# Performance work log

Hardware: AMD Instinct MI355X
Metric: run time of the kernel (lower is better)

The kernel has to match this reference:

```python
import jax, jax.numpy as jnp
import numpy as np

HIDDEN = 2048
N_HEADS = 32
N_KV = 4
HEAD_DIM = 128
EPS = 1e-6
THETA = 1e6
B, S = 2, 2048


def setup_inputs() -> dict:
    key = jax.random.key(0)
    k1, k2, k3 = jax.random.split(key, 3)
    hidden_states = jax.random.normal(k1, (B, S, HIDDEN), dtype=jnp.float32)
    positions = jnp.broadcast_to(jnp.arange(S, dtype=jnp.int32), (B, S))
    w_qkv = jax.random.normal(k2, ((N_HEADS + 2 * N_KV) * HEAD_DIM, HIDDEN), dtype=jnp.float32) * 0.02
    w_o = jax.random.normal(k3, (HIDDEN, N_HEADS * HEAD_DIM), dtype=jnp.float32) * 0.02
    q_norm_w = jnp.ones((HEAD_DIM,), dtype=jnp.float32)
    k_norm_w = jnp.ones((HEAD_DIM,), dtype=jnp.float32)
    return {"hidden_states": hidden_states, "positions": positions,
            "w_qkv": w_qkv, "w_o": w_o, "q_norm_w": q_norm_w, "k_norm_w": k_norm_w}


def _rms_norm(x, w):
    # x: [..., HEAD_DIM]
    var = jnp.mean(x * x, axis=-1, keepdims=True)
    return x * jax.lax.rsqrt(var + EPS) * w


def _rope(x, positions):
    # NEOX-style rotary. x: [B,S,H,D], positions: [B,S]
    half = HEAD_DIM // 2
    inv_freq = 1.0 / (THETA ** (jnp.arange(0, half, dtype=jnp.float32) / half))
    ang = positions.astype(jnp.float32)[..., None] * inv_freq  # [B,S,half]
    cos = jnp.cos(ang)[:, :, None, :]
    sin = jnp.sin(ang)[:, :, None, :]
    x1, x2 = x[..., :half], x[..., half:]
    return jnp.concatenate([x1 * cos - x2 * sin, x2 * cos + x1 * sin], axis=-1)


def reference(hidden_states, positions, w_qkv, w_o, q_norm_w, k_norm_w):
    q_size = N_HEADS * HEAD_DIM
    kv_size = N_KV * HEAD_DIM
    qkv = jnp.einsum('bsh,oh->bso', hidden_states, w_qkv)
    q = qkv[..., :q_size].reshape(B, S, N_HEADS, HEAD_DIM)
    k = qkv[..., q_size:q_size + kv_size].reshape(B, S, N_KV, HEAD_DIM)
    v = qkv[..., q_size + kv_size:].reshape(B, S, N_KV, HEAD_DIM)
    # per-head RMSNorm then RoPE
    q = _rope(_rms_norm(q, q_norm_w), positions)
    k = _rope(_rms_norm(k, k_norm_w), positions)
    rep = N_HEADS // N_KV
    k = jnp.repeat(k, rep, axis=2)
    v = jnp.repeat(v, rep, axis=2)
    scale = HEAD_DIM ** -0.5
    scores = jnp.einsum('bqhd,bkhd->bhqk', q, k) * scale
    causal = jnp.tril(jnp.ones((S, S), dtype=bool))
    scores = jnp.where(causal, scores, jnp.finfo(scores.dtype).min)
    probs = jax.nn.softmax(scores, axis=-1)
    attn = jnp.einsum('bhqk,bkhd->bqhd', probs, v).reshape(B, S, N_HEADS * HEAD_DIM)
    return jnp.einsum('bsa,ha->bsh', attn, w_o)
```

## Files before the change

### kernel.cpp

```cpp
#include <hip/hip_runtime.h>
#include <cstdint>

#define SEQ 2048
#define BATCH 2
#define NTOK 4096
#define HID 2048
#define NH 32
#define NKV 4
#define HD 128
#define QKV_O 5120

typedef __attribute__((ext_vector_type(8))) short short8;
typedef __attribute__((ext_vector_type(8))) unsigned short u16x8;
typedef __attribute__((ext_vector_type(4))) unsigned short u16x4;
typedef __attribute__((ext_vector_type(4))) float f32x4;

__device__ __forceinline__ float bf2f(unsigned short u) {
  union { unsigned int i; float f; } v; v.i = ((unsigned int)u) << 16; return v.f;
}
__device__ __forceinline__ unsigned short f2bf(float f) {
  union { float f; unsigned int i; } v; v.f = f;
  unsigned int r = v.i + 0x7FFFu + ((v.i >> 16) & 1u);
  return (unsigned short)(r >> 16);
}

__device__ __forceinline__ void load_lds16(const void* g, void* l) {
  __builtin_amdgcn_global_load_lds((const __attribute__((address_space(1))) unsigned int*)g,
                                   (__attribute__((address_space(3))) unsigned int*)l, 16, 0, 0);
}

__device__ __forceinline__ float exp2n(float x) { return __builtin_amdgcn_exp2f(x); }

__global__ __launch_bounds__(256) void convert5(
    const float* __restrict__ s0, unsigned short* __restrict__ d0, int n0,
    const float* __restrict__ s1, unsigned short* __restrict__ d1, int n1,
    const float* __restrict__ s2, unsigned short* __restrict__ d2, int n2,
    const float* __restrict__ s3, unsigned short* __restrict__ d3, int n3,
    const float* __restrict__ s4, unsigned short* __restrict__ d4, int n4_) {
  const float* s; unsigned short* d; int n;
  switch (blockIdx.y) {
    case 0: s = s0; d = d0; n = n0; break;
    case 1: s = s1; d = d1; n = n1; break;
    case 2: s = s2; d = d2; n = n2; break;
    case 3: s = s3; d = d3; n = n3; break;
    default: s = s4; d = d4; n = n4_; break;
  }
  int i = blockIdx.x * blockDim.x + threadIdx.x;
  int stride = gridDim.x * blockDim.x;
  for (; i < n; i += stride) {
    f32x4 v = *(const f32x4*)(s + 4 * (size_t)i);
    u16x4 o;
    o.x = f2bf(v.x); o.y = f2bf(v.y); o.z = f2bf(v.z); o.w = f2bf(v.w);
    *(u16x4*)(d + 4 * (size_t)i) = o;
  }
}

template <bool OUT_F32>
__global__ __launch_bounds__(512, 2) void gemm256(
    const unsigned short* __restrict__ A, const unsigned short* __restrict__ B,
    void* __restrict__ Cv, int lda, int ldb, int ldc, int Kloop) {
  __shared__ alignas(16) unsigned short As[2][256 * 64];
  __shared__ alignas(16) unsigned short Bs[2][256 * 64];

  const int t = threadIdx.x;
  const int lane = t & 63, w = t >> 6;
  const int fr = lane & 15, g = lane >> 4;
  const int wm = w >> 2, wn = w & 3;
  const size_t m0 = (size_t)blockIdx.y * 256;
  const size_t n0 = (size_t)blockIdx.x * 256;

  const int srow = w * 8 + (lane >> 3);
  const int sch = (lane & 7) ^ ((lane >> 3) & 7);
  const unsigned short* gA[4];
  const unsigned short* gB[4];
#pragma unroll
  for (int i = 0; i < 4; i++) {
    gA[i] = A + (m0 + i * 64 + srow) * (size_t)lda + sch * 8;
    gB[i] = B + (n0 + i * 64 + srow) * (size_t)ldb + sch * 8;
  }

  auto stage = [&](int k0, int bi) {
#pragma unroll
    for (int i = 0; i < 4; i++) {
      load_lds16(gA[i] + k0, &As[bi][(i * 512 + w * 64) * 8]);
      load_lds16(gB[i] + k0, &Bs[bi][(i * 512 + w * 64) * 8]);
    }
  };

  f32x4 acc[8][4] = {};
  stage(0, 0);

  const int nk = Kloop / 64;
  for (int kt = 0; kt < nk; kt++) {
    const int cur = kt & 1;
    asm volatile("s_waitcnt vmcnt(0)" ::: "memory");
    __builtin_amdgcn_s_barrier();
    __builtin_amdgcn_sched_barrier(0);
    if (kt + 1 < nk) stage((kt + 1) * 64, cur ^ 1);

    const unsigned short* Ac = As[cur];
    const unsigned short* Bc = Bs[cur];

    short8 bfr[4][2];
#pragma unroll
    for (int nf = 0; nf < 4; nf++) {
      const int row = wn * 64 + nf * 16 + fr;
#pragma unroll
      for (int s = 0; s < 2; s++)
        bfr[nf][s] = *(const short8*)&Bc[row * 64 + (((s * 4 + g) ^ (fr & 7)) * 8)];
    }
    __builtin_amdgcn_s_setprio(1);
#pragma unroll
    for (int mf = 0; mf < 8; mf++) {
      const int row = wm * 128 + mf * 16 + fr;
      short8 af0 = *(const short8*)&Ac[row * 64 + (((0 + g) ^ (fr & 7)) * 8)];
      short8 af1 = *(const short8*)&Ac[row * 64 + (((4 + g) ^ (fr & 7)) * 8)];
#pragma unroll
      for (int nf = 0; nf < 4; nf++) {
        acc[mf][nf] = __builtin_amdgcn_mfma_f32_16x16x32_bf16(af0, bfr[nf][0], acc[mf][nf], 0, 0, 0);
        acc[mf][nf] = __builtin_amdgcn_mfma_f32_16x16x32_bf16(af1, bfr[nf][1], acc[mf][nf], 0, 0, 0);
      }
    }
    __builtin_amdgcn_s_setprio(0);
  }

#pragma unroll
  for (int mf = 0; mf < 8; mf++)
#pragma unroll
    for (int nf = 0; nf < 4; nf++) {
      size_t row = m0 + wm * 128 + mf * 16 + g * 4;
      size_t col = n0 + wn * 64 + nf * 16 + fr;
#pragma unroll
      for (int r = 0; r < 4; r++) {
        if (OUT_F32) ((float*)Cv)[(row + r) * ldc + col] = acc[mf][nf][r];
        else ((unsigned short*)Cv)[(row + r) * ldc + col] = f2bf(acc[mf][nf][r]);
      }
    }
}

__global__ __launch_bounds__(512, 2) void gemm256x128(
    const unsigned short* __restrict__ A, const unsigned short* __restrict__ B,
    float* __restrict__ C, int lda, int ldb, int ldc, int Kloop) {
  __shared__ alignas(16) unsigned short As[2][256 * 64];
  __shared__ alignas(16) unsigned short Bs[2][128 * 64];

  const int t = threadIdx.x;
  const int lane = t & 63, w = t >> 6;
  const int fr = lane & 15, g = lane >> 4;
  const int wm = w >> 1, wn = w & 1;
  const size_t m0 = (size_t)blockIdx.y * 256;
  const size_t n0 = (size_t)blockIdx.x * 128;

  const int srow = t >> 3;
  const int sch = (t & 7) ^ ((t >> 3) & 7);
  const unsigned short* gA[4];
  const unsigned short* gB[2];
#pragma unroll
  for (int i = 0; i < 4; i++)
    gA[i] = A + (m0 + i * 64 + srow) * (size_t)lda + sch * 8;
#pragma unroll
  for (int i = 0; i < 2; i++)
    gB[i] = B + (n0 + i * 64 + srow) * (size_t)ldb + sch * 8;

  auto stage = [&](int k0, int bi) {
#pragma unroll
    for (int i = 0; i < 4; i++)
      load_lds16(gA[i] + k0, &As[bi][(i * 512 + w * 64) * 8]);
#pragma unroll
    for (int i = 0; i < 2; i++)
      load_lds16(gB[i] + k0, &Bs[bi][(i * 512 + w * 64) * 8]);
  };

  f32x4 acc[4][4] = {};
  stage(0, 0);

  const int nk = Kloop / 64;
  for (int kt = 0; kt < nk; kt++) {
    const int cur = kt & 1;
    asm volatile("s_waitcnt vmcnt(0)" ::: "memory");
    __builtin_amdgcn_s_barrier();
    __builtin_amdgcn_sched_barrier(0);
    if (kt + 1 < nk) stage((kt + 1) * 64, cur ^ 1);

    const unsigned short* Ac = As[cur];
    const unsigned short* Bc = Bs[cur];

    short8 bfr[4][2];
#pragma unroll
    for (int nf = 0; nf < 4; nf++) {
      const int row = wn * 64 + nf * 16 + fr;
#pragma unroll
      for (int s = 0; s < 2; s++)
        bfr[nf][s] = *(const short8*)&Bc[row * 64 + (((s * 4 + g) ^ (fr & 7)) * 8)];
    }
    __builtin_amdgcn_s_setprio(1);
#pragma unroll
    for (int mf = 0; mf < 4; mf++) {
      const int row = wm * 64 + mf * 16 + fr;
      short8 af0 = *(const short8*)&Ac[row * 64 + (((0 + g) ^ (fr & 7)) * 8)];
      short8 af1 = *(const short8*)&Ac[row * 64 + (((4 + g) ^ (fr & 7)) * 8)];
#pragma unroll
      for (int nf = 0; nf < 4; nf++) {
        acc[mf][nf] = __builtin_amdgcn_mfma_f32_16x16x32_bf16(af0, bfr[nf][0], acc[mf][nf], 0, 0, 0);
        acc[mf][nf] = __builtin_amdgcn_mfma_f32_16x16x32_bf16(af1, bfr[nf][1], acc[mf][nf], 0, 0, 0);
      }
    }
    __builtin_amdgcn_s_setprio(0);
  }

#pragma unroll
  for (int mf = 0; mf < 4; mf++)
#pragma unroll
    for (int nf = 0; nf < 4; nf++) {
      size_t row = m0 + wm * 64 + mf * 16 + g * 4;
      size_t col = n0 + wn * 64 + nf * 16 + fr;
#pragma unroll
      for (int r = 0; r < 4; r++)
        C[(row + r) * ldc + col] = acc[mf][nf][r];
    }
}

template <bool OUT_F32>
__global__ __launch_bounds__(256) void gemm_bt_bf16(
    const unsigned short* __restrict__ A, const unsigned short* __restrict__ B,
    void* __restrict__ Cv, int lda, int ldb, int ldc, int K) {
  __shared__ alignas(16) unsigned short As[128 * 32];
  __shared__ alignas(16) unsigned short Bs[128 * 32];

  const int t    = threadIdx.x;
  const int lane = t & 63;
  const int w    = t >> 6;
  const int wm   = (w >> 1) * 64;
  const int wn   = (w & 1) * 64;
  const size_t m0 = (size_t)blockIdx.y * 128;
  const size_t n0 = (size_t)blockIdx.x * 128;

  f32x4 acc[4][4] = {};

  const int srow = w * 32 + (lane >> 2);
  const int scol = (lane & 3) * 8;
  const unsigned short* gA0 = &A[(m0 + srow) * (size_t)lda + scol];
  const unsigned short* gA1 = gA0 + 16 * (size_t)lda;
  const unsigned short* gB0 = &B[(n0 + srow) * (size_t)ldb + scol];
  const unsigned short* gB1 = gB0 + 16 * (size_t)ldb;
  unsigned short* lA0 = &As[(w * 32) * 32];
  unsigned short* lA1 = &As[(w * 32 + 16) * 32];
  unsigned short* lB0 = &Bs[(w * 32) * 32];
  unsigned short* lB1 = &Bs[(w * 32 + 16) * 32];

  const int fr = lane & 15;
  const int kb = (lane >> 4) * 8;

  for (int k0 = 0; k0 < K; k0 += 32) {
    load_lds16(gA0 + k0, lA0);
    load_lds16(gA1 + k0, lA1);
    load_lds16(gB0 + k0, lB0);
    load_lds16(gB1 + k0, lB1);
    __syncthreads();
    short8 af[4], bf[4];
#pragma unroll
    for (int mt = 0; mt < 4; mt++) af[mt] = *(const short8*)&As[(wm + mt * 16 + fr) * 32 + kb];
#pragma unroll
    for (int nt = 0; nt < 4; nt++) bf[nt] = *(const short8*)&Bs[(wn + nt * 16 + fr) * 32 + kb];
#pragma unroll
    for (int mt = 0; mt < 4; mt++)
#pragma unroll
      for (int nt = 0; nt < 4; nt++)
        acc[mt][nt] = __builtin_amdgcn_mfma_f32_16x16x32_bf16(af[mt], bf[nt], acc[mt][nt], 0, 0, 0);
    __syncthreads();
  }

  const int r4 = (lane >> 4) * 4;
  const int cc = lane & 15;
#pragma unroll
  for (int mt = 0; mt < 4; mt++)
#pragma unroll
    for (int nt = 0; nt < 4; nt++) {
      size_t row = m0 + wm + mt * 16 + r4;
      size_t col = n0 + wn + nt * 16 + cc;
#pragma unroll
      for (int r = 0; r < 4; r++) {
        if (OUT_F32) ((float*)Cv)[(row + r) * ldc + col] = acc[mt][nt][r];
        else ((unsigned short*)Cv)[(row + r) * ldc + col] = f2bf(acc[mt][nt][r]);
      }
    }
}

__global__ __launch_bounds__(64) void rope_tab(const int* __restrict__ pos,
                                               float2* __restrict__ tab) {
  const int tok = blockIdx.x;
  const int j = threadIdx.x;
  float p = (float)pos[tok];
  float inv_freq = expf((float)j * (-13.815510557964274f / 64.0f));
  float ang = p * inv_freq;
  float2 cs; cs.x = cosf(ang); cs.y = sinf(ang);
  tab[tok * 64 + j] = cs;
}

__global__ __launch_bounds__(256) void normrope_tv(
    unsigned short* __restrict__ qkv, const float2* __restrict__ tab,
    const unsigned short* __restrict__ qw, const unsigned short* __restrict__ kw,
    unsigned short* __restrict__ vt) {
  __shared__ alignas(16) unsigned short Vs[64][136];
  const int bid = blockIdx.x;
  const int t = threadIdx.x;

  if (bid < 9 * NTOK) {
    const int wv = t >> 6, lane = t & 63;
    const int hh = bid % 9;
    const int tok = bid / 9;
    const int h = hh * 4 + wv;
    const unsigned short* w = (h < NH) ? qw : kw;
    const size_t src = (size_t)tok * QKV_O + (size_t)h * HD;

    float x1 = bf2f(qkv[src + lane]);
    float x2 = bf2f(qkv[src + lane + 64]);
    float ss = x1 * x1 + x2 * x2;
#pragma unroll
    for (int off = 32; off; off >>= 1) ss += __shfl_xor(ss, off);
    float r = rsqrtf(ss * (1.0f / 128.0f) + 1e-6f);
    float n1 = x1 * r * bf2f(w[lane]);
    float n2 = x2 * r * bf2f(w[lane + 64]);

    float2 cs = tab[tok * 64 + lane];
    qkv[src + lane]      = f2bf(n1 * cs.x - n2 * cs.y);
    qkv[src + lane + 64] = f2bf(n2 * cs.x + n1 * cs.y);
  } else {
    const int r = bid - 9 * NTOK;
    const int tile = r & 31, kvh = (r >> 5) & 3, b = r >> 7;
    const int k0 = tile * 64;
    const int voff = (NH + NKV) * HD + kvh * HD;
    {
      const int row = t >> 2, cb = (t & 3) * 8;
      const size_t gb = (size_t)(b * SEQ + k0 + row) * QKV_O + voff;
#pragma unroll
      for (int i = 0; i < 4; i++)
        *(uint4*)&Vs[row][cb + 32 * i] = *(const uint4*)&qkv[gb + cb + 32 * i];
    }
    __syncthreads();
    const int d = t >> 1, half = t & 1;
    const size_t ob = ((size_t)((b * NKV + kvh) * HD + d)) * SEQ + k0 + half * 32;
#pragma unroll
    for (int i = 0; i < 4; i++) {
      u16x8 vv;
#pragma unroll
      for (int j = 0; j < 8; j++) vv[j] = Vs[half * 32 + i * 8 + j][d];
      *(u16x8*)&vt[ob + i * 8] = vv;
    }
  }
}

__global__ __launch_bounds__(512, 4) void flash_mfma(unsigned short* __restrict__ qkv,
                                                     const unsigned short* __restrict__ vt) {
  __shared__ alignas(16) unsigned short Kbuf[2][64 * 128];
  __shared__ alignas(16) unsigned short Vbuf[2][128 * 64];
  __shared__ alignas(16) unsigned short Ps[8][16 * 64];

  const int p = (int)blockIdx.x;
  const int h = blockIdx.y, b = blockIdx.z;
  const int t = threadIdx.x;
  const int lane = t & 63, w = t >> 6;
  const int c = lane & 15, g = lane >> 4;
  const int kvh = h >> 3;
  const int koff = NH * HD + kvh * HD;
  const float scale2 = 0.12751745f;
  const int swz = c & 7;
  const int nqt = SEQ / 128;

  const int rK0 = t >> 4,         jK0 = (t & 15) ^ (rK0 & 15);
  const int rK1 = (t + 512) >> 4, jK1 = ((t + 512) & 15) ^ (rK1 & 15);
  const int dV0 = t >> 3,         jV0 = (t & 7) ^ (dV0 & 7);
  const int dV1 = (t + 512) >> 3, jV1 = ((t + 512) & 7) ^ (dV1 & 7);
  const unsigned short* gK0 = qkv + (size_t)(b * SEQ + rK0) * QKV_O + koff + jK0 * 8;
  const unsigned short* gK1 = qkv + (size_t)(b * SEQ + rK1) * QKV_O + koff + jK1 * 8;
  const unsigned short* gV0 = vt + ((size_t)(b * NKV + kvh) * HD + dV0) * SEQ + jV0 * 8;
  const unsigned short* gV1 = vt + ((size_t)(b * NKV + kvh) * HD + dV1) * SEQ + jV1 * 8;

  auto stage = [&](int k0s, int bi) {
    load_lds16(gK0 + (size_t)k0s * QKV_O, &Kbuf[bi][(w * 64) * 8]);
    load_lds16(gK1 + (size_t)k0s * QKV_O, &Kbuf[bi][(w * 64 + 512) * 8]);
    load_lds16(gV0 + k0s, &Vbuf[bi][(w * 64) * 8]);
    load_lds16(gV1 + k0s, &Vbuf[bi][(w * 64 + 512) * 8]);
  };

  for (int job = 0; job < 2; job++) {
    const int qt = job == 0 ? (nqt - 1 - p) : p;
    const int q0 = qt * 128;
    const int nkt = 2 * qt + 2;

    stage(0, 0);

    short8 qf[4];
    {
      const size_t qr = (size_t)(b * SEQ + q0 + w * 16 + c) * QKV_O + (size_t)h * HD;
#pragma unroll
      for (int ks = 0; ks < 4; ks++)
        qf[ks] = *(const short8*)&qkv[qr + ks * 32 + g * 8];
    }

    f32x4 O[8] = {};
    float m_i = -1e30f, l_i = 0.0f;

    for (int kt = 0; kt < nkt; kt++) {
      const int cur = kt & 1;
      asm volatile("s_waitcnt vmcnt(0)" ::: "memory");
      __builtin_amdgcn_s_barrier();
      __builtin_amdgcn_sched_barrier(0);
      if (kt + 1 < nkt) stage((kt + 1) * 64, cur ^ 1);

      const unsigned short* Kc = Kbuf[cur];
      const unsigned short* Vc = Vbuf[cur];

      f32x4 sc[4];
#pragma unroll
      for (int mt = 0; mt < 4; mt++) sc[mt] = (f32x4){0.f, 0.f, 0.f, 0.f};
      __builtin_amdgcn_s_setprio(1);
#pragma unroll
      for (int ks = 0; ks < 4; ks++) {
#pragma unroll
        for (int mt = 0; mt < 4; mt++) {
          short8 kf = *(const short8*)&Kc[(mt * 16 + c) * 128 + (((ks * 4 + g) ^ c) * 8)];
          sc[mt] = __builtin_amdgcn_mfma_f32_16x16x32_bf16(kf, qf[ks], sc[mt], 0, 0, 0);
        }
      }
      __builtin_amdgcn_s_setprio(0);

      const int k0 = kt * 64;
      const int qrow = q0 + w * 16 + c;
      const bool need_mask = (k0 + 63 > q0 + w * 16);
#pragma unroll
      for (int mt = 0; mt < 4; mt++)
#pragma unroll
        for (int r = 0; r < 4; r++) {
          float s = sc[mt][r];
          if (need_mask && (k0 + mt * 16 + g * 4 + r > qrow)) s = -3.0e38f;
          sc[mt][r] = s;
        }
      float ma = fmaxf(fmaxf(sc[0][0], sc[0][1]), sc[0][2]);
      float mb = fmaxf(fmaxf(sc[0][3], sc[1][0]), sc[1][1]);
      float mc = fmaxf(fmaxf(sc[1][2], sc[1][3]), sc[2][0]);
      float md = fmaxf(fmaxf(sc[2][1], sc[2][2]), sc[2][3]);
      float me = fmaxf(fmaxf(sc[3][0], sc[3][1]), sc[3][2]);
      float mx = fmaxf(fmaxf(fmaxf(ma, mb), fmaxf(mc, md)), fmaxf(me, sc[3][3]));
      mx = fmaxf(mx, __shfl_xor(mx, 16));
      mx = fmaxf(mx, __shfl_xor(mx, 32));
      float mx2 = mx * scale2;

      if (!__all(mx2 - m_i <= 11.54156f)) {
        float m_new = fmaxf(m_i, mx2);
        float alpha = exp2n(m_i - m_new);
        f32x4 a4;
#pragma unroll
        for (int r = 0; r < 4; r++) a4[r] = __shfl(alpha, g * 4 + r);
#pragma unroll
        for (int nt = 0; nt < 8; nt++)
#pragma unroll
          for (int r = 0; r < 4; r++) O[nt][r] *= a4[r];
        l_i *= alpha;
        m_i = m_new;
      }

      float psum = 0.0f;
#pragma unroll
      for (int mt = 0; mt < 4; mt++) {
        float pv[4];
#pragma unroll
        for (int r = 0; r < 4; r++) {
          pv[r] = exp2n(__builtin_fmaf(sc[mt][r], scale2, -m_i));
          psum += pv[r];
        }
        unsigned int pk0, pk1;
        asm("v_cvt_pk_bf16_f32 %0, %1, %2" : "=v"(pk0) : "v"(pv[0]), "v"(pv[1]));
        asm("v_cvt_pk_bf16_f32 %0, %1, %2" : "=v"(pk1) : "v"(pv[2]), "v"(pv[3]));
        uint2 pk; pk.x = pk0; pk.y = pk1;
        *(uint2*)&Ps[w][c * 64 + (((mt * 2 + (g >> 1)) ^ swz) * 8) + (g & 1) * 4] = pk;
      }
      psum += __shfl_xor(psum, 16);
      psum += __shfl_xor(psum, 32);
      l_i += psum;

      __builtin_amdgcn_s_setprio(1);
#pragma unroll
      for (int ks = 0; ks < 2; ks++) {
        short8 pf = *(const short8*)&Ps[w][c * 64 + (((ks * 4 + g) ^ swz) * 8)];
#pragma unroll
        for (int nt = 0; nt < 8; nt++) {
          short8 vf = *(const short8*)&Vc[(nt * 16 + c) * 64 + (((ks * 4 + g) ^ swz) * 8)];
          O[nt] = __builtin_amdgcn_mfma_f32_16x16x32_bf16(pf, vf, O[nt], 0, 0, 0);
        }
      }
      __builtin_amdgcn_s_setprio(0);
    }

    f32x4 l4;
#pragma unroll
    for (int r = 0; r < 4; r++) l4[r] = __shfl(l_i, g * 4 + r);
    f32x4 li;
#pragma unroll
    for (int r = 0; r < 4; r++) li[r] = 1.0f / l4[r];
#pragma unroll
    for (int nt = 0; nt < 8; nt++)
#pragma unroll
      for (int r = 0; r < 4; r++) {
        size_t addr = (size_t)(b * SEQ + q0 + w * 16 + g * 4 + r) * QKV_O + h * HD + nt * 16 + c;
        qkv[addr] = f2bf(O[nt][r] * li[r]);
      }
  }
}

extern "C" void kernel_launch(void* const* d_in, const int* in_sizes, int n_in,
                              void* d_out, int out_size, void* d_ws, size_t ws_size,
                              hipStream_t stream) {
  const float* hidden_f = (const float*)d_in[0];
  const int* positions  = (const int*)d_in[1];
  const float* wqkv_f   = (const float*)d_in[2];
  const float* wo_f     = (const float*)d_in[3];
  const float* qn_f     = (const float*)d_in[4];
  const float* kn_f     = (const float*)d_in[5];
  float* out            = (float*)d_out;

  char* ws = (char*)d_ws;
  unsigned short* hidden_c = (unsigned short*)ws;
  unsigned short* wqkv_c   = (unsigned short*)(ws + 16777216);
  unsigned short* wo_c     = (unsigned short*)(ws + 37748736);
  unsigned short* qn_c     = (unsigned short*)(ws + 54525952);
  unsigned short* kn_c     = (unsigned short*)(ws + 54526208);
  unsigned short* qkv      = (unsigned short*)(ws + 54526464);
  unsigned short* vt_g     = (unsigned short*)(ws + 96469504);
  float2* rtab             = (float2*)ws;

  convert5<<<dim3(512, 5), 256, 0, stream>>>(
      hidden_f, hidden_c, NTOK * HID / 4,
      wqkv_f, wqkv_c, QKV_O * HID / 4,
      wo_f, wo_c, HID * NH * HD / 4,
      qn_f, qn_c, HD / 4,
      kn_f, kn_c, HD / 4);

  gemm256<false><<<dim3(NH * HD / 256, NTOK / 256), 512, 0, stream>>>(
      hidden_c, wqkv_c, qkv, HID, HID, QKV_O, HID);
  gemm_bt_bf16<false><<<dim3(2 * NKV * HD / 128, NTOK / 128), 256, 0, stream>>>(
      hidden_c, wqkv_c + (size_t)(NH * HD) * HID, qkv + NH * HD, HID, HID, QKV_O, HID);
  rope_tab<<<NTOK, 64, 0, stream>>>(positions, rtab);
  normrope_tv<<<9 * NTOK + 256, 256, 0, stream>>>(qkv, rtab, qn_c, kn_c, vt_g);
  flash_mfma<<<dim3(SEQ / 256, NH, BATCH), 512, 0, stream>>>(qkv, vt_g);
  gemm256x128<<<dim3(HID / 128, NTOK / 256), 512, 0, stream>>>(
      qkv, wo_c, out, QKV_O, NH * HD, HID, NH * HD);
}
```

Baseline: 464.7 us.

## Shrink flash KV tile to 32 and launch one q-tile per block

The flash attention kernel drops the paired-job scheme, where each block handled a long and a short causal q-tile. It now launches one block per 128-row q-tile, ordered longest first, and halves the K/V tile from 64 to 32 keys. LDS use shrinks enough that the launch bounds now ask for 8 blocks per CU instead of 4, which may raise occupancy and shorten per-step latency. In exchange it pays twice as many barriers and loop iterations, loses the load balancing the pairing gave, and may face register pressure under the tighter bound.

```diff
diff --git a/kernel.cpp b/kernel.cpp
--- a/kernel.cpp
+++ b/kernel.cpp
@@ -350,13 +350,13 @@
   }
 }
 
-__global__ __launch_bounds__(512, 4) void flash_mfma(unsigned short* __restrict__ qkv,
+__global__ __launch_bounds__(512, 8) void flash_mfma(unsigned short* __restrict__ qkv,
                                                      const unsigned short* __restrict__ vt) {
-  __shared__ alignas(16) unsigned short Kbuf[2][64 * 128];
-  __shared__ alignas(16) unsigned short Vbuf[2][128 * 64];
-  __shared__ alignas(16) unsigned short Ps[8][16 * 64];
-
-  const int p = (int)blockIdx.x;
+  __shared__ alignas(16) unsigned short Kbuf[2][32 * 128];
+  __shared__ alignas(16) unsigned short Vbuf[2][128 * 32];
+  __shared__ alignas(16) unsigned short Ps[8][16 * 32];
+
+  const int qt = 15 - (int)blockIdx.x;
   const int h = blockIdx.y, b = blockIdx.z;
   const int t = threadIdx.x;
   const int lane = t & 63, w = t >> 6;
@@ -364,148 +364,133 @@
   const int kvh = h >> 3;
   const int koff = NH * HD + kvh * HD;
   const float scale2 = 0.12751745f;
-  const int swz = c & 7;
-  const int nqt = SEQ / 128;
-
-  const int rK0 = t >> 4,         jK0 = (t & 15) ^ (rK0 & 15);
-  const int rK1 = (t + 512) >> 4, jK1 = ((t + 512) & 15) ^ (rK1 & 15);
-  const int dV0 = t >> 3,         jV0 = (t & 7) ^ (dV0 & 7);
-  const int dV1 = (t + 512) >> 3, jV1 = ((t + 512) & 7) ^ (dV1 & 7);
-  const unsigned short* gK0 = qkv + (size_t)(b * SEQ + rK0) * QKV_O + koff + jK0 * 8;
-  const unsigned short* gK1 = qkv + (size_t)(b * SEQ + rK1) * QKV_O + koff + jK1 * 8;
-  const unsigned short* gV0 = vt + ((size_t)(b * NKV + kvh) * HD + dV0) * SEQ + jV0 * 8;
-  const unsigned short* gV1 = vt + ((size_t)(b * NKV + kvh) * HD + dV1) * SEQ + jV1 * 8;
+  const int swz3 = c & 3;
+  const int q0 = qt * 128;
+  const int nkt = 4 * qt + 4;
+
+  const int rK = t >> 4, jK = (t & 15) ^ (rK & 15);
+  const int dV = t >> 2, jV = (t & 3) ^ (dV & 3);
+  const unsigned short* gK = qkv + (size_t)(b * SEQ + rK) * QKV_O + koff + jK * 8;
+  const unsigned short* gV = vt + ((size_t)(b * NKV + kvh) * HD + dV) * SEQ + jV * 8;
 
   auto stage = [&](int k0s, int bi) {
-    load_lds16(gK0 + (size_t)k0s * QKV_O, &Kbuf[bi][(w * 64) * 8]);
-    load_lds16(gK1 + (size_t)k0s * QKV_O, &Kbuf[bi][(w * 64 + 512) * 8]);
-    load_lds16(gV0 + k0s, &Vbuf[bi][(w * 64) * 8]);
-    load_lds16(gV1 + k0s, &Vbuf[bi][(w * 64 + 512) * 8]);
+    load_lds16(gK + (size_t)k0s * QKV_O, &Kbuf[bi][(w * 64) * 8]);
+    load_lds16(gV + k0s, &Vbuf[bi][(w * 64) * 8]);
   };
 
-  for (int job = 0; job < 2; job++) {
-    const int qt = job == 0 ? (nqt - 1 - p) : p;
-    const int q0 = qt * 128;
-    const int nkt = 2 * qt + 2;
-
-    stage(0, 0);
-
-    short8 qf[4];
+  stage(0, 0);
+
+  short8 qf[4];
+  {
+    const size_t qr = (size_t)(b * SEQ + q0 + w * 16 + c) * QKV_O + (size_t)h * HD;
+#pragma unroll
+    for (int ks = 0; ks < 4; ks++)
+      qf[ks] = *(const short8*)&qkv[qr + ks * 32 + g * 8];
+  }
+
+  f32x4 O[8] = {};
+  float m_i = -1e30f, l_i = 0.0f;
+
+  for (int kt = 0; kt < nkt; kt++) {
+    const int cur = kt & 1;
+    asm volatile("s_waitcnt vmcnt(0)" ::: "memory");
+    __builtin_amdgcn_s_barrier();
+    __builtin_amdgcn_sched_barrier(0);
+    if (kt + 1 < nkt) stage((kt + 1) * 32, cur ^ 1);
+
+    const unsigned short* Kc = Kbuf[cur];
+    const unsigned short* Vc = Vbuf[cur];
+
+    f32x4 sc[2];
+#pragma unroll
+    for (int mt = 0; mt < 2; mt++) sc[mt] = (f32x4){0.f, 0.f, 0.f, 0.f};
+    __builtin_amdgcn_s_setprio(1);
+#pragma unroll
+    for (int ks = 0; ks < 4; ks++) {
+#pragma unroll
+      for (int mt = 0; mt < 2; mt++) {
+        short8 kf = *(const short8*)&Kc[(mt * 16 + c) * 128 + (((ks * 4 + g) ^ c) * 8)];
+        sc[mt] = __builtin_amdgcn_mfma_f32_16x16x32_bf16(kf, qf[ks], sc[mt], 0, 0, 0);
+      }
+    }
+    __builtin_amdgcn_s_setprio(0);
+
+    const int k0 = kt * 32;
+    const int qrow = q0 + w * 16 + c;
+    const bool need_mask = (k0 + 31 > q0 + w * 16);
+#pragma unroll
+    for (int mt = 0; mt < 2; mt++)
+#pragma unroll
+      for (int r = 0; r < 4; r++) {
+        float s = sc[mt][r];
+        if (need_mask && (k0 + mt * 16 + g * 4 + r > qrow)) s = -3.0e38f;
+        sc[mt][r] = s;
+      }
+    float ma = fmaxf(fmaxf(sc[0][0], sc[0][1]), sc[0][2]);
+    float mb = fmaxf(fmaxf(sc[0][3], sc[1][0]), sc[1][1]);
+    float mx = fmaxf(fmaxf(ma, mb), fmaxf(sc[1][2], sc[1][3]));
+    mx = fmaxf(mx, __shfl_xor(mx, 16));
+    mx = fmaxf(mx, __shfl_xor(mx, 32));
+    float mx2 = mx * scale2;
+
+    if (!__all(mx2 - m_i <= 11.54156f)) {
+      float m_new = fmaxf(m_i, mx2);
+      float alpha = exp2n(m_i - m_new);
+      f32x4 a4;
+#pragma unroll
+      for (int r = 0; r < 4; r++) a4[r] = __shfl(alpha, g * 4 + r);
+#pragma unroll
+      for (int nt = 0; nt < 8; nt++)
+#pragma unroll
+        for (int r = 0; r < 4; r++) O[nt][r] *= a4[r];
+      l_i *= alpha;
+      m_i = m_new;
+    }
+
+    float psum = 0.0f;
+#pragma unroll
+    for (int mt = 0; mt < 2; mt++) {
+      float pv[4];
+#pragma unroll
+      for (int r = 0; r < 4; r++) {
+        pv[r] = exp2n(__builtin_fmaf(sc[mt][r], scale2, -m_i));
+        psum += pv[r];
+      }
+      unsigned int pk0, pk1;
+      asm("v_cvt_pk_bf16_f32 %0, %1, %2" : "=v"(pk0) : "v"(pv[0]), "v"(pv[1]));
+      asm("v_cvt_pk_bf16_f32 %0, %1, %2" : "=v"(pk1) : "v"(pv[2]), "v"(pv[3]));
+      uint2 pk; pk.x = pk0; pk.y = pk1;
+      *(uint2*)&Ps[w][c * 32 + (((mt * 2 + (g >> 1)) ^ swz3) * 8) + (g & 1) * 4] = pk;
+    }
+    psum += __shfl_xor(psum, 16);
+    psum += __shfl_xor(psum, 32);
+    l_i += psum;
+
+    __builtin_amdgcn_s_setprio(1);
     {
-      const size_t qr = (size_t)(b * SEQ + q0 + w * 16 + c) * QKV_O + (size_t)h * HD;
-#pragma unroll
-      for (int ks = 0; ks < 4; ks++)
-        qf[ks] = *(const short8*)&qkv[qr + ks * 32 + g * 8];
-    }
-
-    f32x4 O[8] = {};
-    float m_i = -1e30f, l_i = 0.0f;
-
-    for (int kt = 0; kt < nkt; kt++) {
-      const int cur = kt & 1;
-      asm volatile("s_waitcnt vmcnt(0)" ::: "memory");
-      __builtin_amdgcn_s_barrier();
-      __builtin_amdgcn_sched_barrier(0);
-      if (kt + 1 < nkt) stage((kt + 1) * 64, cur ^ 1);
-
-      const unsigned short* Kc = Kbuf[cur];
-      const unsigned short* Vc = Vbuf[cur];
-
-      f32x4 sc[4];
-#pragma unroll
-      for (int mt = 0; mt < 4; mt++) sc[mt] = (f32x4){0.f, 0.f, 0.f, 0.f};
-      __builtin_amdgcn_s_setprio(1);
-#pragma unroll
-      for (int ks = 0; ks < 4; ks++) {
-#pragma unroll
-        for (int mt = 0; mt < 4; mt++) {
-          short8 kf = *(const short8*)&Kc[(mt * 16 + c) * 128 + (((ks * 4 + g) ^ c) * 8)];
-          sc[mt] = __builtin_amdgcn_mfma_f32_16x16x32_bf16(kf, qf[ks], sc[mt], 0, 0, 0);
-        }
-      }
-      __builtin_amdgcn_s_setprio(0);
-
-      const int k0 = kt * 64;
-      const int qrow = q0 + w * 16 + c;
-      const bool need_mask = (k0 + 63 > q0 + w * 16);
-#pragma unroll
-      for (int mt = 0; mt < 4; mt++)
-#pragma unroll
-        for (int r = 0; r < 4; r++) {
-          float s = sc[mt][r];
-          if (need_mask && (k0 + mt * 16 + g * 4 + r > qrow)) s = -3.0e38f;
-          sc[mt][r] = s;
-        }
-      float ma = fmaxf(fmaxf(sc[0][0], sc[0][1]), sc[0][2]);
-      float mb = fmaxf(fmaxf(sc[0][3], sc[1][0]), sc[1][1]);
-      float mc = fmaxf(fmaxf(sc[1][2], sc[1][3]), sc[2][0]);
-      float md = fmaxf(fmaxf(sc[2][1], sc[2][2]), sc[2][3]);
-      float me = fmaxf(fmaxf(sc[3][0], sc[3][1]), sc[3][2]);
-      float mx = fmaxf(fmaxf(fmaxf(ma, mb), fmaxf(mc, md)), fmaxf(me, sc[3][3]));
-      mx = fmaxf(mx, __shfl_xor(mx, 16));
-      mx = fmaxf(mx, __shfl_xor(mx, 32));
-      float mx2 = mx * scale2;
-
-      if (!__all(mx2 - m_i <= 11.54156f)) {
-        float m_new = fmaxf(m_i, mx2);
-        float alpha = exp2n(m_i - m_new);
-        f32x4 a4;
-#pragma unroll
-        for (int r = 0; r < 4; r++) a4[r] = __shfl(alpha, g * 4 + r);
-#pragma unroll
-        for (int nt = 0; nt < 8; nt++)
-#pragma unroll
-          for (int r = 0; r < 4; r++) O[nt][r] *= a4[r];
-        l_i *= alpha;
-        m_i = m_new;
-      }
-
-      float psum = 0.0f;
-#pragma unroll
-      for (int mt = 0; mt < 4; mt++) {
-        float pv[4];
-#pragma unroll
-        for (int r = 0; r < 4; r++) {
-          pv[r] = exp2n(__builtin_fmaf(sc[mt][r], scale2, -m_i));
-          psum += pv[r];
-        }
-        unsigned int pk0, pk1;
-        asm("v_cvt_pk_bf16_f32 %0, %1, %2" : "=v"(pk0) : "v"(pv[0]), "v"(pv[1]));
-        asm("v_cvt_pk_bf16_f32 %0, %1, %2" : "=v"(pk1) : "v"(pv[2]), "v"(pv[3]));
-        uint2 pk; pk.x = pk0; pk.y = pk1;
-        *(uint2*)&Ps[w][c * 64 + (((mt * 2 + (g >> 1)) ^ swz) * 8) + (g & 1) * 4] = pk;
-      }
-      psum += __shfl_xor(psum, 16);
-      psum += __shfl_xor(psum, 32);
-      l_i += psum;
-
-      __builtin_amdgcn_s_setprio(1);
-#pragma unroll
-      for (int ks = 0; ks < 2; ks++) {
-        short8 pf = *(const short8*)&Ps[w][c * 64 + (((ks * 4 + g) ^ swz) * 8)];
-#pragma unroll
-        for (int nt = 0; nt < 8; nt++) {
-          short8 vf = *(const short8*)&Vc[(nt * 16 + c) * 64 + (((ks * 4 + g) ^ swz) * 8)];
-          O[nt] = __builtin_amdgcn_mfma_f32_16x16x32_bf16(pf, vf, O[nt], 0, 0, 0);
-        }
-      }
-      __builtin_amdgcn_s_setprio(0);
-    }
-
-    f32x4 l4;
-#pragma unroll
-    for (int r = 0; r < 4; r++) l4[r] = __shfl(l_i, g * 4 + r);
-    f32x4 li;
-#pragma unroll
-    for (int r = 0; r < 4; r++) li[r] = 1.0f / l4[r];
-#pragma unroll
-    for (int nt = 0; nt < 8; nt++)
-#pragma unroll
-      for (int r = 0; r < 4; r++) {
-        size_t addr = (size_t)(b * SEQ + q0 + w * 16 + g * 4 + r) * QKV_O + h * HD + nt * 16 + c;
-        qkv[addr] = f2bf(O[nt][r] * li[r]);
-      }
-  }
+      short8 pf = *(const short8*)&Ps[w][c * 32 + ((g ^ swz3) * 8)];
+#pragma unroll
+      for (int nt = 0; nt < 8; nt++) {
+        short8 vf = *(const short8*)&Vc[(nt * 16 + c) * 32 + ((g ^ swz3) * 8)];
+        O[nt] = __builtin_amdgcn_mfma_f32_16x16x32_bf16(pf, vf, O[nt], 0, 0, 0);
+      }
+    }
+    __builtin_amdgcn_s_setprio(0);
+  }
+
+  f32x4 l4;
+#pragma unroll
+  for (int r = 0; r < 4; r++) l4[r] = __shfl(l_i, g * 4 + r);
+  f32x4 li;
+#pragma unroll
+  for (int r = 0; r < 4; r++) li[r] = 1.0f / l4[r];
+#pragma unroll
+  for (int nt = 0; nt < 8; nt++)
+#pragma unroll
+    for (int r = 0; r < 4; r++) {
+      size_t addr = (size_t)(b * SEQ + q0 + w * 16 + g * 4 + r) * QKV_O + h * HD + nt * 16 + c;
+      qkv[addr] = f2bf(O[nt][r] * li[r]);
+    }
 }
 
 extern "C" void kernel_launch(void* const* d_in, const int* in_sizes, int n_in,
@@ -542,7 +527,7 @@
       hidden_c, wqkv_c + (size_t)(NH * HD) * HID, qkv + NH * HD, HID, HID, QKV_O, HID);
   rope_tab<<<NTOK, 64, 0, stream>>>(positions, rtab);
   normrope_tv<<<9 * NTOK + 256, 256, 0, stream>>>(qkv, rtab, qn_c, kn_c, vt_g);
-  flash_mfma<<<dim3(SEQ / 256, NH, BATCH), 512, 0, stream>>>(qkv, vt_g);
+  flash_mfma<<<dim3(SEQ / 128, NH, BATCH), 512, 0, stream>>>(qkv, vt_g);
   gemm256x128<<<dim3(HID / 128, NTOK / 256), 512, 0, stream>>>(
       qkv, wo_c, out, QKV_O, NH * HD, HID, NH * HD);
 }
```

New measurement: 778.9 us. 1.68x slower.
